# Performance work log

Hardware: AMD Instinct MI355X
Metric: run time of the kernel (lower is better)

The kernel has to match this reference:

```python
import jax, jax.numpy as jnp
import numpy as np

RESERVOIR = 8192
INPUT_SIZE = 3
OUTPUT_SIZE = 3
PRED_LEN = 512
SPECTRAL_RADIUS = 0.9
SPARSITY = 0.1


def setup_inputs() -> dict:
    key = jax.random.key(0)
    k1, k2, k3, k4, k5 = jax.random.split(key, 5)
    x = jax.random.normal(k1, (1, PRED_LEN, INPUT_SIZE), dtype=jnp.float32)
    Win = jax.random.normal(k2, (RESERVOIR, INPUT_SIZE), dtype=jnp.float32)
    # Sparse reservoir matrix scaled to target spectral radius.
    # Circular law: spectral radius of N(0,1)*Bernoulli(p) mask ~ sqrt(N*p),
    # used here in place of the exact eigvals-based rescale in __init__.
    W = jax.random.normal(k3, (RESERVOIR, RESERVOIR), dtype=jnp.float32)
    mask = (jax.random.uniform(k4, (RESERVOIR, RESERVOIR)) < SPARSITY).astype(jnp.float32)
    W = W * mask * (SPECTRAL_RADIUS / np.sqrt(RESERVOIR * SPARSITY))
    Wout_w = jax.random.normal(k5, (OUTPUT_SIZE, RESERVOIR), dtype=jnp.float32) / np.sqrt(RESERVOIR)
    Wout_b = jnp.zeros((OUTPUT_SIZE,), dtype=jnp.float32)
    return {"x": x, "Win": Win, "W": W, "Wout_w": Wout_w, "Wout_b": Wout_b}


def reference(x, Win, W, Wout_w, Wout_b):
    # x: [1, T, input_size], T >= PRED_LEN so every step is teacher-forced
    xs = x[0, :PRED_LEN, :]  # [T, input_size]

    def step(h, xt):
        h_new = jnp.tanh(Win @ xt + W @ h)
        y = Wout_w @ h_new + Wout_b  # [output_size]
        return h_new, y

    h0 = jnp.zeros((RESERVOIR,), dtype=x.dtype)
    _, ys = jax.lax.scan(step, h0, xs)  # ys: [PRED_LEN, output_size]
    return ys[None, :, :]  # [1, PRED_LEN, output_size] == x[:, -pred_len:, :]
```

## Files before the change

kernel.cpp:

```cpp
#include <hip/hip_runtime.h>
#include <hip/hip_fp16.h>
#include <stdint.h>

#define RES 8192
#define TSTEPS 512
#define NB 256
#define NT 512
#define ROWS_PER_BLOCK 32
#define LPR 16
#define SLOTS 72
#define PW_ITERS (SLOTS / 4)
#define ROW_DW (SLOTS * LPR)
#define NGROUP 8
#define GSTRIDE 16

#define WS_PACKED_OFF   0u
#define WS_H16_OFF      37748736u
#define WS_FLAGS_OFF    (37748736u + 8404992u)

__global__ __launch_bounds__(256) void esn_compress(const float* __restrict__ W,
                                                    uint32_t* __restrict__ packed) {
    __shared__ uint32_t lst[4][1024];
    __shared__ uint32_t grid[4][LPR][SLOTS];
    __shared__ unsigned exc_s[4][32];
    __shared__ unsigned tbase_s[4][32];

    const int wave = threadIdx.x >> 6;
    const int lane = threadIdx.x & 63;
    const int row  = blockIdx.x * 4 + wave;
    const float* wrow = W + (size_t)row * RES;
    uint32_t* prow = packed + (size_t)row * ROW_DW;

    unsigned nnz = 0;
    for (int chunk = 0; chunk < RES / 64; ++chunk) {
        const int c = chunk * 64 + lane;
        const float v = wrow[c];
        const bool nz = (v != 0.0f);
        const unsigned long long m = __ballot(nz);
        if (nz) {
            unsigned pos = nnz + (unsigned)__popcll(m & ((1ull << lane) - 1ull));
            if (pos < 1024u) {
                uint32_t b = (__float_as_uint(v) + 0x1000u) & 0xFFFFE000u;
                lst[wave][pos] = b | (uint32_t)c;
            }
        }
        nnz += (unsigned)__popcll(m);
    }
    if (nnz > 1024u) nnz = 1024u;
    __syncthreads();

    for (int d = lane; d < LPR * SLOTS; d += 64) {
        const int li = d / SLOTS;
        const int sl = d % SLOTS;
        const unsigned rot = (((unsigned)row & 1u) << 4) | (unsigned)li;
        grid[wave][li][sl] = (sl < 64) ? ((rot + (unsigned)sl) & 31u) : 0u;
    }
    __syncthreads();

    if (lane < 32) {
        unsigned cb = 0;
        for (unsigned idx = 0; idx < nnz; ++idx)
            cb += ((lst[wave][idx] & 31u) == (unsigned)lane) ? 1u : 0u;
        exc_s[wave][lane] = (cb > 32u) ? (cb - 32u) : 0u;
    }
    __syncthreads();
    if (lane == 0) {
        unsigned run = 0;
        for (int b2 = 0; b2 < 32; ++b2) { tbase_s[wave][b2] = run; run += exc_s[wave][b2]; }
    }
    __syncthreads();

    if (lane < 32) {
        const unsigned b = (unsigned)lane;
        const unsigned tb = tbase_s[wave][lane];
        unsigned i = 0;
        for (unsigned idx = 0; idx < nnz; ++idx) {
            const uint32_t e = lst[wave][idx];
            if ((e & 31u) == b) {
                if (i < 32u) {
                    const unsigned li = i & 15u;
                    const unsigned j  = i >> 4;
                    const unsigned rot = (((unsigned)row & 1u) << 4) | li;
                    const unsigned s = j * 32u + ((b - rot) & 31u);
                    grid[wave][li][s] = e;
                } else {
                    const unsigned q = tb + (i - 32u);
                    if (q < 128u) grid[wave][q & 15u][64u + (q >> 4)] = e;
                }
                ++i;
            }
        }
    }
    __syncthreads();

    for (int d = lane; d < ROW_DW; d += 64) {
        const int li = (d & 63) >> 2;
        const int sl = ((d >> 6) << 2) | (d & 3);
        prow[d] = grid[wave][li][sl];
    }
}

__device__ __forceinline__ float2 unpack_h2(unsigned u) {
    __half2 h = *reinterpret_cast<__half2*>(&u);
    return __half22float2(h);
}

__global__ __launch_bounds__(NT) void esn_loop(const float* __restrict__ x,
                                               const float* __restrict__ Win,
                                               const float* __restrict__ Wout_w,
                                               const float* __restrict__ Wout_b,
                                               const uint32_t* __restrict__ packed,
                                               uint32_t* __restrict__ h16,
                                               unsigned* __restrict__ flags,
                                               float* __restrict__ out) {
    __shared__ float lds_h[RES];
    __shared__ float lds_hnew[ROWS_PER_BLOCK];
    __shared__ float lds_red[NT / 64][3];
    __shared__ float lds_x[TSTEPS * 3];

    const int tid = threadIdx.x;
    const int bid = blockIdx.x;
    const int li  = tid & (LPR - 1);
    const int rlocal = tid >> 4;
    const int row = bid * ROWS_PER_BLOCK + rlocal;
    const bool leader = (li == 0);
    const int grp = bid & (NGROUP - 1);

    __builtin_amdgcn_fence(__ATOMIC_ACQUIRE, "agent");

    for (int i = tid; i < TSTEPS * 3; i += NT) lds_x[i] = x[i];

    uint4 pw[PW_ITERS];
    {
        const uint4* prow = ((const uint4*)packed) + (size_t)row * (ROW_DW / 4);
#pragma unroll
        for (int i = 0; i < PW_ITERS; ++i) pw[i] = prow[i * LPR + li];
    }

    float win0 = 0.f, win1 = 0.f, win2 = 0.f;
    if (leader) {
        win0 = Win[row * 3 + 0];
        win1 = Win[row * 3 + 1];
        win2 = Win[row * 3 + 2];
    }
    __syncthreads();

    float4* const lds4 = (float4*)lds_h;

    for (int t = 0; t < TSTEPS; ++t) {
        float bias = 0.f;
        if (leader)
            bias = win0 * lds_x[t * 3 + 0] + win1 * lds_x[t * 3 + 1] + win2 * lds_x[t * 3 + 2];

        if (t == 0) {
            const float4 z4 = make_float4(0.f, 0.f, 0.f, 0.f);
            for (int i = tid; i < RES / 4; i += NT) lds4[i] = z4;
            __syncthreads();
        } else {
            if (tid < NGROUP) {
                const unsigned target = (unsigned)t * (NB / NGROUP);
                while (__hip_atomic_load(&flags[tid * GSTRIDE], __ATOMIC_RELAXED,
                                         __HIP_MEMORY_SCOPE_AGENT) < target) {
                    __builtin_amdgcn_s_sleep(1);
                }
            }
            __syncthreads();
            const uint2* src = (const uint2*)(h16 + (size_t)t * (RES / 2));
#pragma unroll
            for (int k = 0; k < 4; ++k) {
                const int j = tid + k * NT;
                const uint2 e = src[j];
                const float2 f0 = unpack_h2(e.x);
                const float2 f1 = unpack_h2(e.y);
                lds4[j] = make_float4(f0.x, f0.y, f1.x, f1.y);
            }
            __syncthreads();
        }

        float a0 = 0.f, a1 = 0.f, a2 = 0.f, a3 = 0.f;
#pragma unroll
        for (int i = 0; i < PW_ITERS; ++i) {
            const uint4 p = pw[i];
            a0 += __uint_as_float(p.x & 0xFFFFE000u) * lds_h[p.x & 8191u];
            a1 += __uint_as_float(p.y & 0xFFFFE000u) * lds_h[p.y & 8191u];
            a2 += __uint_as_float(p.z & 0xFFFFE000u) * lds_h[p.z & 8191u];
            a3 += __uint_as_float(p.w & 0xFFFFE000u) * lds_h[p.w & 8191u];
        }
        float acc = (a0 + a1) + (a2 + a3);
#pragma unroll
        for (int off = LPR / 2; off >= 1; off >>= 1)
            acc += __shfl_xor(acc, off, LPR);

        if (leader) lds_hnew[rlocal] = tanhf(acc + bias);
        __syncthreads();

        if (tid < 16) {
            __half2 hp = __floats2half2_rn(lds_hnew[tid * 2], lds_hnew[tid * 2 + 1]);
            const unsigned pk = *reinterpret_cast<unsigned*>(&hp);
            __hip_atomic_store(&h16[(size_t)(t + 1) * (RES / 2) + bid * 16 + tid], pk,
                               __ATOMIC_RELAXED, __HIP_MEMORY_SCOPE_AGENT);
        }
        __syncthreads();
        if (tid == 0) {
            asm volatile("s_waitcnt vmcnt(0)" ::: "memory");
            __hip_atomic_fetch_add(&flags[grp * GSTRIDE], 1u,
                                   __ATOMIC_RELAXED, __HIP_MEMORY_SCOPE_AGENT);
        }
    }

    if (tid < NGROUP) {
        const unsigned target = (unsigned)TSTEPS * (NB / NGROUP);
        while (__hip_atomic_load(&flags[tid * GSTRIDE], __ATOMIC_RELAXED,
                                 __HIP_MEMORY_SCOPE_AGENT) < target) {
            __builtin_amdgcn_s_sleep(1);
        }
    }
    __syncthreads();

    const float b0 = Wout_b[0], b1 = Wout_b[1], b2 = Wout_b[2];
    for (int pass = 0; pass < TSTEPS / NB; ++pass) {
        const int tout = bid * (TSTEPS / NB) + pass;
        __syncthreads();
        {
            const uint2* src = (const uint2*)(h16 + (size_t)(tout + 1) * (RES / 2));
#pragma unroll
            for (int k = 0; k < 4; ++k) {
                const int j = tid + k * NT;
                const uint2 e = src[j];
                const float2 f0 = unpack_h2(e.x);
                const float2 f1 = unpack_h2(e.y);
                lds4[j] = make_float4(f0.x, f0.y, f1.x, f1.y);
            }
        }
        __syncthreads();
        float s0 = 0.f, s1 = 0.f, s2 = 0.f;
        for (int i = tid; i < RES; i += NT) {
            const float hv = lds_h[i];
            s0 += Wout_w[i] * hv;
            s1 += Wout_w[RES + i] * hv;
            s2 += Wout_w[2 * RES + i] * hv;
        }
#pragma unroll
        for (int off = 32; off >= 1; off >>= 1) {
            s0 += __shfl_xor(s0, off, 64);
            s1 += __shfl_xor(s1, off, 64);
            s2 += __shfl_xor(s2, off, 64);
        }
        const int wv = tid >> 6;
        if ((tid & 63) == 0) { lds_red[wv][0] = s0; lds_red[wv][1] = s1; lds_red[wv][2] = s2; }
        __syncthreads();
        if (tid < 3) {
            float sum = 0.f;
            for (int w = 0; w < NT / 64; ++w) sum += lds_red[w][tid];
            out[tout * 3 + tid] = sum + (tid == 0 ? b0 : (tid == 1 ? b1 : b2));
        }
    }
}

extern "C" void kernel_launch(void* const* d_in, const int* in_sizes, int n_in,
                              void* d_out, int out_size, void* d_ws, size_t ws_size,
                              hipStream_t stream) {
    const float* x      = (const float*)d_in[0];
    const float* Win    = (const float*)d_in[1];
    const float* W      = (const float*)d_in[2];
    const float* Wout_w = (const float*)d_in[3];
    const float* Wout_b = (const float*)d_in[4];

    uint8_t* ws = (uint8_t*)d_ws;
    uint32_t* packed = (uint32_t*)(ws + WS_PACKED_OFF);
    uint32_t* h16    = (uint32_t*)(ws + WS_H16_OFF);
    unsigned* flags  = (unsigned*)(ws + WS_FLAGS_OFF);
    float*    out    = (float*)d_out;

    (void)hipMemsetAsync(flags, 0, 1024, stream);
    esn_compress<<<dim3(RES / 4), dim3(256), 0, stream>>>(W, packed);

    void* args[] = { (void*)&x, (void*)&Win, (void*)&Wout_w, (void*)&Wout_b,
                     (void*)&packed, (void*)&h16, (void*)&flags, (void*)&out };
    (void)hipLaunchCooperativeKernel((void*)esn_loop, dim3(NB), dim3(NT), args, 0u, stream);
}
```

Measured before the change: 2.206 ms.

## Replace grouped flag counters with per-element step-tagged hidden state polling

Drops the atomic flag counters and the barrier plus waitcnt handshake between time steps. Each hidden-state element is now stored as a 32-bit word holding the fp16 value and a step tag, and consumers poll each word until its tag matches the current step. The intent is to remove a serialized release/acquire round trip per step so consumers read data as soon as it lands. In exchange the state buffer doubles in size, a larger memset is needed, and polling traffic on the loads grows. The weight mask in the inner loop is also dropped, so the low index bits now feed into the weight value.

```diff
diff --git a/kernel.cpp b/kernel.cpp
--- a/kernel.cpp
+++ b/kernel.cpp
@@ -11,12 +11,11 @@
 #define SLOTS 72
 #define PW_ITERS (SLOTS / 4)
 #define ROW_DW (SLOTS * LPR)
-#define NGROUP 8
-#define GSTRIDE 16
+#define HWT (RES / NT)
 
 #define WS_PACKED_OFF   0u
-#define WS_H16_OFF      37748736u
-#define WS_FLAGS_OFF    (37748736u + 8404992u)
+#define WS_HSEQ_OFF     37748736u
+#define HSEQ_BYTES      16809984u
 
 __global__ __launch_bounds__(256) void esn_compress(const float* __restrict__ W,
                                                     uint32_t* __restrict__ packed) {
@@ -100,18 +99,12 @@
     }
 }
 
-__device__ __forceinline__ float2 unpack_h2(unsigned u) {
-    __half2 h = *reinterpret_cast<__half2*>(&u);
-    return __half22float2(h);
-}
-
 __global__ __launch_bounds__(NT) void esn_loop(const float* __restrict__ x,
                                                const float* __restrict__ Win,
                                                const float* __restrict__ Wout_w,
                                                const float* __restrict__ Wout_b,
                                                const uint32_t* __restrict__ packed,
-                                               uint32_t* __restrict__ h16,
-                                               unsigned* __restrict__ flags,
+                                               uint32_t* __restrict__ hseq,
                                                float* __restrict__ out) {
     __shared__ float lds_h[RES];
     __shared__ float lds_hnew[ROWS_PER_BLOCK];
@@ -124,7 +117,6 @@
     const int rlocal = tid >> 4;
     const int row = bid * ROWS_PER_BLOCK + rlocal;
     const bool leader = (li == 0);
-    const int grp = bid & (NGROUP - 1);
 
     __builtin_amdgcn_fence(__ATOMIC_ACQUIRE, "agent");
 
@@ -155,36 +147,37 @@
         if (t == 0) {
             const float4 z4 = make_float4(0.f, 0.f, 0.f, 0.f);
             for (int i = tid; i < RES / 4; i += NT) lds4[i] = z4;
-            __syncthreads();
         } else {
-            if (tid < NGROUP) {
-                const unsigned target = (unsigned)t * (NB / NGROUP);
-                while (__hip_atomic_load(&flags[tid * GSTRIDE], __ATOMIC_RELAXED,
-                                         __HIP_MEMORY_SCOPE_AGENT) < target) {
-                    __builtin_amdgcn_s_sleep(1);
+            const uint32_t* src = hseq + (size_t)t * RES;
+            const unsigned tt = (unsigned)t;
+            uint32_t vals[HWT];
+            unsigned pend = 0xFFFFu;
+            do {
+#pragma unroll
+                for (int k = 0; k < HWT; ++k) {
+                    if (pend & (1u << k)) {
+                        const uint32_t e = __hip_atomic_load(&src[tid + k * NT],
+                                             __ATOMIC_RELAXED, __HIP_MEMORY_SCOPE_AGENT);
+                        if ((e >> 16) == tt) { vals[k] = e; pend &= ~(1u << k); }
+                    }
                 }
-            }
-            __syncthreads();
-            const uint2* src = (const uint2*)(h16 + (size_t)t * (RES / 2));
-#pragma unroll
-            for (int k = 0; k < 4; ++k) {
-                const int j = tid + k * NT;
-                const uint2 e = src[j];
-                const float2 f0 = unpack_h2(e.x);
-                const float2 f1 = unpack_h2(e.y);
-                lds4[j] = make_float4(f0.x, f0.y, f1.x, f1.y);
-            }
-            __syncthreads();
-        }
+                if (pend) __builtin_amdgcn_s_sleep(1);
+            } while (pend);
+#pragma unroll
+            for (int k = 0; k < HWT; ++k)
+                lds_h[tid + k * NT] =
+                    __half2float(__ushort_as_half((unsigned short)(vals[k] & 0xFFFFu)));
+        }
+        __syncthreads();
 
         float a0 = 0.f, a1 = 0.f, a2 = 0.f, a3 = 0.f;
 #pragma unroll
         for (int i = 0; i < PW_ITERS; ++i) {
             const uint4 p = pw[i];
-            a0 += __uint_as_float(p.x & 0xFFFFE000u) * lds_h[p.x & 8191u];
-            a1 += __uint_as_float(p.y & 0xFFFFE000u) * lds_h[p.y & 8191u];
-            a2 += __uint_as_float(p.z & 0xFFFFE000u) * lds_h[p.z & 8191u];
-            a3 += __uint_as_float(p.w & 0xFFFFE000u) * lds_h[p.w & 8191u];
+            a0 += __uint_as_float(p.x) * lds_h[p.x & 8191u];
+            a1 += __uint_as_float(p.y) * lds_h[p.y & 8191u];
+            a2 += __uint_as_float(p.z) * lds_h[p.z & 8191u];
+            a3 += __uint_as_float(p.w) * lds_h[p.w & 8191u];
         }
         float acc = (a0 + a1) + (a2 + a3);
 #pragma unroll
@@ -194,43 +187,38 @@
         if (leader) lds_hnew[rlocal] = tanhf(acc + bias);
         __syncthreads();
 
-        if (tid < 16) {
-            __half2 hp = __floats2half2_rn(lds_hnew[tid * 2], lds_hnew[tid * 2 + 1]);
-            const unsigned pk = *reinterpret_cast<unsigned*>(&hp);
-            __hip_atomic_store(&h16[(size_t)(t + 1) * (RES / 2) + bid * 16 + tid], pk,
+        if (tid < ROWS_PER_BLOCK) {
+            const __half hh = __float2half_rn(lds_hnew[tid]);
+            const uint32_t pk = ((uint32_t)(t + 1) << 16) | (uint32_t)__half_as_ushort(hh);
+            __hip_atomic_store(&hseq[(size_t)(t + 1) * RES + bid * ROWS_PER_BLOCK + tid], pk,
                                __ATOMIC_RELAXED, __HIP_MEMORY_SCOPE_AGENT);
         }
-        __syncthreads();
-        if (tid == 0) {
-            asm volatile("s_waitcnt vmcnt(0)" ::: "memory");
-            __hip_atomic_fetch_add(&flags[grp * GSTRIDE], 1u,
-                                   __ATOMIC_RELAXED, __HIP_MEMORY_SCOPE_AGENT);
-        }
-    }
-
-    if (tid < NGROUP) {
-        const unsigned target = (unsigned)TSTEPS * (NB / NGROUP);
-        while (__hip_atomic_load(&flags[tid * GSTRIDE], __ATOMIC_RELAXED,
-                                 __HIP_MEMORY_SCOPE_AGENT) < target) {
-            __builtin_amdgcn_s_sleep(1);
-        }
-    }
-    __syncthreads();
+    }
 
     const float b0 = Wout_b[0], b1 = Wout_b[1], b2 = Wout_b[2];
     for (int pass = 0; pass < TSTEPS / NB; ++pass) {
         const int tout = bid * (TSTEPS / NB) + pass;
         __syncthreads();
         {
-            const uint2* src = (const uint2*)(h16 + (size_t)(tout + 1) * (RES / 2));
-#pragma unroll
-            for (int k = 0; k < 4; ++k) {
-                const int j = tid + k * NT;
-                const uint2 e = src[j];
-                const float2 f0 = unpack_h2(e.x);
-                const float2 f1 = unpack_h2(e.y);
-                lds4[j] = make_float4(f0.x, f0.y, f1.x, f1.y);
-            }
+            const uint32_t* src = hseq + (size_t)(tout + 1) * RES;
+            const unsigned tt = (unsigned)(tout + 1);
+            uint32_t vals[HWT];
+            unsigned pend = 0xFFFFu;
+            do {
+#pragma unroll
+                for (int k = 0; k < HWT; ++k) {
+                    if (pend & (1u << k)) {
+                        const uint32_t e = __hip_atomic_load(&src[tid + k * NT],
+                                             __ATOMIC_RELAXED, __HIP_MEMORY_SCOPE_AGENT);
+                        if ((e >> 16) == tt) { vals[k] = e; pend &= ~(1u << k); }
+                    }
+                }
+                if (pend) __builtin_amdgcn_s_sleep(1);
+            } while (pend);
+#pragma unroll
+            for (int k = 0; k < HWT; ++k)
+                lds_h[tid + k * NT] =
+                    __half2float(__ushort_as_half((unsigned short)(vals[k] & 0xFFFFu)));
         }
         __syncthreads();
         float s0 = 0.f, s1 = 0.f, s2 = 0.f;
@@ -268,14 +256,13 @@
 
     uint8_t* ws = (uint8_t*)d_ws;
     uint32_t* packed = (uint32_t*)(ws + WS_PACKED_OFF);
-    uint32_t* h16    = (uint32_t*)(ws + WS_H16_OFF);
-    unsigned* flags  = (unsigned*)(ws + WS_FLAGS_OFF);
+    uint32_t* hseq   = (uint32_t*)(ws + WS_HSEQ_OFF);
     float*    out    = (float*)d_out;
 
-    (void)hipMemsetAsync(flags, 0, 1024, stream);
+    (void)hipMemsetAsync(hseq, 0, HSEQ_BYTES, stream);
     esn_compress<<<dim3(RES / 4), dim3(256), 0, stream>>>(W, packed);
 
     void* args[] = { (void*)&x, (void*)&Win, (void*)&Wout_w, (void*)&Wout_b,
-                     (void*)&packed, (void*)&h16, (void*)&flags, (void*)&out };
+                     (void*)&packed, (void*)&hseq, (void*)&out };
     (void)hipLaunchCooperativeKernel((void*)esn_loop, dim3(NB), dim3(NT), args, 0u, stream);
 }
```

After: 3.430 ms. +55.5%, slower.
